# Kernel tuning notes

Hardware: AMD Instinct MI355X
Metric: run time of the kernel (lower is better)

## Reference

```python
import jax, jax.numpy as jnp
import numpy as np

EPS = 1e-6  # torch.nn.CosineSimilarity eps


def setup_inputs() -> dict:
    key = jax.random.key(0)
    k1, k2, k3, k4 = jax.random.split(key, 4)
    B, S, I, H, P = 16, 512, 512, 512, 16
    hidden = jax.random.normal(k1, (B, S, I), dtype=jnp.float32)
    # per-prototype linear weights (no bias); torch Linear stores (out, in)
    W1 = jax.random.normal(k2, (P, H, I), dtype=jnp.float32) / np.sqrt(I)
    W2 = jax.random.normal(k3, (P, H, H), dtype=jnp.float32) / np.sqrt(H)
    protos = jax.random.normal(k4, (P, H), dtype=jnp.float32)  # torch.randn(1,H) per proto
    return {"hidden": hidden, "W1": W1, "W2": W2, "protos": protos}


def reference(hidden, W1, W2, protos):
    # Batched version of the per-prototype loop:
    # layer1: ReLU(hidden @ W1[p].T) -> [B,S,P,H]
    h1 = jax.nn.relu(jnp.einsum("bsi,phi->bsph", hidden, W1))
    # layer2: ReLU(h1 @ W2[p].T) -> [B,S,P,H]
    h2 = jax.nn.relu(jnp.einsum("bsph,pgh->bspg", h1, W2))
    # cosine similarity along feature dim vs. each prototype vector
    dot = jnp.einsum("bsph,ph->bsp", h2, protos)
    xn = jnp.maximum(jnp.linalg.norm(h2, axis=-1), EPS)          # [B,S,P]
    pn = jnp.maximum(jnp.linalg.norm(protos, axis=-1), EPS)      # [P]
    cos_scores = dot / (xn * pn)                                  # [B,S,P]
    return cos_scores
```

## Files before the change

kernel.cpp:

```cpp
#include <hip/hip_runtime.h>
#include <hip/hip_bf16.h>

#define R_TOT 8192
#define DIM   512
#define NP    16
#define EPSV  1e-6f

typedef __bf16 bf16x8 __attribute__((ext_vector_type(8)));
typedef float  f32x16 __attribute__((ext_vector_type(16)));

__device__ __forceinline__ unsigned int f2bf(float f) {
  unsigned int u = __float_as_uint(f);
  return (u + 0x7FFFu + ((u >> 16) & 1u)) >> 16;
}
__device__ __forceinline__ unsigned int pack2(float a, float b) {
  return f2bf(a) | (f2bf(b) << 16);
}
__device__ __forceinline__ f32x16 zero16() {
  f32x16 z;
  #pragma unroll
  for (int i = 0; i < 16; ++i) z[i] = 0.f;
  return z;
}

__global__ void cvt_x_kernel(const float* __restrict__ X, unsigned short* __restrict__ Xb) {
  int t   = blockIdx.x * 256 + threadIdx.x;
  int row = t >> 6;
  int c   = t & 63;
  const float4* src = (const float4*)(X + (size_t)row * DIM + c * 8);
  float4 f0 = src[0], f1 = src[1];
  uint4 o;
  o.x = pack2(f0.x, f0.y);
  o.y = pack2(f0.z, f0.w);
  o.z = pack2(f1.x, f1.y);
  o.w = pack2(f1.z, f1.w);
  *(uint4*)(Xb + (size_t)row * DIM + 8 * (c ^ (row & 7))) = o;
}

__global__ void pack_w_kernel(const float* __restrict__ W, unsigned short* __restrict__ Wp) {
  int t  = blockIdx.x * 256 + threadIdx.x;
  int l  = t & 63;
  int kk = (t >> 6) & 31;
  int mt = (t >> 11) & 15;
  int p  = t >> 15;
  int row = mt * 32 + (l & 31);
  int k0  = 16 * kk + 8 * (l >> 5);
  const float4* s = (const float4*)(W + ((size_t)p * DIM + row) * DIM + k0);
  float4 f0 = s[0], f1 = s[1];
  uint4 o;
  o.x = pack2(f0.x, f0.y);
  o.y = pack2(f0.z, f0.w);
  o.z = pack2(f1.x, f1.y);
  o.w = pack2(f1.z, f1.w);
  *(uint4*)(Wp + (size_t)t * 8) = o;
}

__global__ void proto_norm_kernel(const float* __restrict__ protos, float* __restrict__ pn) {
  int p = blockIdx.x;
  int l = threadIdx.x;
  float ss = 0.f;
  #pragma unroll
  for (int k = 0; k < DIM / 64; ++k) {
    float v = protos[p * DIM + k * 64 + l];
    ss += v * v;
  }
  #pragma unroll
  for (int m = 32; m >= 1; m >>= 1) ss += __shfl_xor(ss, m, 64);
  if (l == 0) pn[p] = fmaxf(sqrtf(ss), EPSV);
}

__device__ __forceinline__ void gemm_stage32(const unsigned short* tile,
                                             const unsigned short* __restrict__ Wpk,
                                             f32x16 acc[2],
                                             int l, int l31, int h) {
  #pragma unroll
  for (int kk = 0; kk < 32; ++kk) {
    bf16x8 a = *(const bf16x8*)(Wpk + kk * 512 + l * 8);
    #pragma unroll
    for (int nt = 0; nt < 2; ++nt) {
      int token = nt * 32 + l31;
      int boff  = (32 * kk + 16 * h) ^ ((token & 7) << 4);
      bf16x8 b = *(const bf16x8*)((const char*)tile + token * 1024 + boff);
      acc[nt] = __builtin_amdgcn_mfma_f32_32x32x16_bf16(a, b, acc[nt], 0, 0, 0);
    }
  }
}

__global__ __launch_bounds__(1024) void fused_kernel(
    const unsigned short* __restrict__ Xb,
    const unsigned short* __restrict__ W1p,
    const unsigned short* __restrict__ W2p,
    const float* __restrict__ protos,
    const float* __restrict__ pn,
    float* __restrict__ out) {
  __shared__ unsigned short tile[64 * DIM];
  __shared__ float red[16][64][2];

  const int raw = blockIdx.x;
  const int bid = (raw & 7) * 256 + (raw >> 3);
  const int p   = bid >> 7;
  const int r0  = (bid & 127) << 6;
  const int tid = threadIdx.x;
  const int w   = tid >> 6;
  const int l   = tid & 63;
  const int l31 = l & 31;
  const int h   = l >> 5;

  {
    const uint4* g = (const uint4*)(Xb + (size_t)r0 * DIM);
    uint4* s = (uint4*)tile;
    #pragma unroll
    for (int it = 0; it < 4; ++it) s[tid + it * 1024] = g[tid + it * 1024];
  }
  __syncthreads();

  f32x16 acc[2];
  acc[0] = zero16();
  acc[1] = zero16();

  gemm_stage32(tile, W1p + ((size_t)p * 16 + w) * 16384, acc, l, l31, h);

  __syncthreads();

  #pragma unroll
  for (int nt = 0; nt < 2; ++nt) {
    int token = nt * 32 + l31;
    #pragma unroll
    for (int g = 0; g < 4; ++g) {
      uint2 pk;
      pk.x = pack2(fmaxf(acc[nt][4 * g + 0], 0.f), fmaxf(acc[nt][4 * g + 1], 0.f));
      pk.y = pack2(fmaxf(acc[nt][4 * g + 2], 0.f), fmaxf(acc[nt][4 * g + 3], 0.f));
      int featb = 64 * w + 16 * g + 8 * h;
      *(uint2*)((char*)tile + token * 1024 + (featb ^ ((token & 7) << 4))) = pk;
    }
  }
  __syncthreads();

  acc[0] = zero16();
  acc[1] = zero16();

  gemm_stage32(tile, W2p + ((size_t)p * 16 + w) * 16384, acc, l, l31, h);

  float4 pv[4];
  #pragma unroll
  for (int g = 0; g < 4; ++g)
    pv[g] = *(const float4*)(protos + p * DIM + 32 * w + 8 * g + 4 * h);

  #pragma unroll
  for (int nt = 0; nt < 2; ++nt) {
    float d = 0.f, ssq = 0.f;
    #pragma unroll
    for (int g = 0; g < 4; ++g)
      #pragma unroll
      for (int j = 0; j < 4; ++j) {
        float hv = fmaxf(acc[nt][4 * g + j], 0.f);
        d   += hv * ((const float*)&pv[g])[j];
        ssq += hv * hv;
      }
    d   += __shfl_xor(d, 32, 64);
    ssq += __shfl_xor(ssq, 32, 64);
    if (l < 32) {
      red[w][nt * 32 + l31][0] = d;
      red[w][nt * 32 + l31][1] = ssq;
    }
  }
  __syncthreads();

  if (tid < 64) {
    float d = 0.f, ssq = 0.f;
    #pragma unroll
    for (int ww = 0; ww < 16; ++ww) {
      d   += red[ww][tid][0];
      ssq += red[ww][tid][1];
    }
    float xn = fmaxf(sqrtf(ssq), EPSV);
    out[(size_t)(r0 + tid) * NP + p] = d / (xn * pn[p]);
  }
}

extern "C" void kernel_launch(void* const* d_in, const int* in_sizes, int n_in,
                              void* d_out, int out_size, void* d_ws, size_t ws_size,
                              hipStream_t stream) {
  const float* X      = (const float*)d_in[0];
  const float* W1     = (const float*)d_in[1];
  const float* W2     = (const float*)d_in[2];
  const float* protos = (const float*)d_in[3];
  float* out = (float*)d_out;

  unsigned short* Xb  = (unsigned short*)d_ws;
  unsigned short* W1p = Xb  + (size_t)R_TOT * DIM;
  unsigned short* W2p = W1p + (size_t)NP * DIM * DIM;
  float* pn = (float*)(W2p + (size_t)NP * DIM * DIM);

  cvt_x_kernel<<<2048, 256, 0, stream>>>(X, Xb);
  pack_w_kernel<<<2048, 256, 0, stream>>>(W1, W1p);
  pack_w_kernel<<<2048, 256, 0, stream>>>(W2, W2p);
  proto_norm_kernel<<<NP, 64, 0, stream>>>(protos, pn);
  fused_kernel<<<2048, 1024, 0, stream>>>(Xb, W1p, W2p, protos, pn, out);
}
```

Measured before the change: 177.2 us.

## Halve fused block to 512 threads with 2x2 MFMA tiles per wave

Each wave now computes two 32-row output tiles instead of one, so every B fragment read from shared memory feeds two MFMAs and LDS traffic per MFMA drops. The block shrinks from 16 to 8 waves, with launch bounds of 512 threads and a minimum of 4 blocks. The k-loop is no longer force-unrolled. Each thread now holds four accumulators, which raises register pressure and can limit occupancy. The reduction buffer shrinks to match the smaller block.

```diff
diff --git a/kernel.cpp b/kernel.cpp
--- a/kernel.cpp
+++ b/kernel.cpp
@@ -71,22 +71,28 @@
 
 __device__ __forceinline__ void gemm_stage32(const unsigned short* tile,
                                              const unsigned short* __restrict__ Wpk,
-                                             f32x16 acc[2],
+                                             f32x16 acc[2][2],
                                              int l, int l31, int h) {
-  #pragma unroll
   for (int kk = 0; kk < 32; ++kk) {
-    bf16x8 a = *(const bf16x8*)(Wpk + kk * 512 + l * 8);
+    bf16x8 a[2], b[2];
+    #pragma unroll
+    for (int mi = 0; mi < 2; ++mi)
+      a[mi] = *(const bf16x8*)(Wpk + (size_t)mi * 16384 + kk * 512 + l * 8);
     #pragma unroll
     for (int nt = 0; nt < 2; ++nt) {
       int token = nt * 32 + l31;
       int boff  = (32 * kk + 16 * h) ^ ((token & 7) << 4);
-      bf16x8 b = *(const bf16x8*)((const char*)tile + token * 1024 + boff);
-      acc[nt] = __builtin_amdgcn_mfma_f32_32x32x16_bf16(a, b, acc[nt], 0, 0, 0);
-    }
-  }
-}
-
-__global__ __launch_bounds__(1024) void fused_kernel(
+      b[nt] = *(const bf16x8*)((const char*)tile + token * 1024 + boff);
+    }
+    #pragma unroll
+    for (int mi = 0; mi < 2; ++mi)
+      #pragma unroll
+      for (int nt = 0; nt < 2; ++nt)
+        acc[mi][nt] = __builtin_amdgcn_mfma_f32_32x32x16_bf16(a[mi], b[nt], acc[mi][nt], 0, 0, 0);
+  }
+}
+
+__global__ __launch_bounds__(512, 4) void fused_kernel(
     const unsigned short* __restrict__ Xb,
     const unsigned short* __restrict__ W1p,
     const unsigned short* __restrict__ W2p,
@@ -94,7 +100,7 @@
     const float* __restrict__ pn,
     float* __restrict__ out) {
   __shared__ unsigned short tile[64 * DIM];
-  __shared__ float red[16][64][2];
+  __shared__ float red[8][64][2];
 
   const int raw = blockIdx.x;
   const int bid = (raw & 7) * 256 + (raw >> 3);
@@ -110,52 +116,57 @@
     const uint4* g = (const uint4*)(Xb + (size_t)r0 * DIM);
     uint4* s = (uint4*)tile;
     #pragma unroll
-    for (int it = 0; it < 4; ++it) s[tid + it * 1024] = g[tid + it * 1024];
-  }
-  __syncthreads();
-
-  f32x16 acc[2];
-  acc[0] = zero16();
-  acc[1] = zero16();
-
-  gemm_stage32(tile, W1p + ((size_t)p * 16 + w) * 16384, acc, l, l31, h);
-
-  __syncthreads();
-
-  #pragma unroll
-  for (int nt = 0; nt < 2; ++nt) {
-    int token = nt * 32 + l31;
-    #pragma unroll
-    for (int g = 0; g < 4; ++g) {
-      uint2 pk;
-      pk.x = pack2(fmaxf(acc[nt][4 * g + 0], 0.f), fmaxf(acc[nt][4 * g + 1], 0.f));
-      pk.y = pack2(fmaxf(acc[nt][4 * g + 2], 0.f), fmaxf(acc[nt][4 * g + 3], 0.f));
-      int featb = 64 * w + 16 * g + 8 * h;
-      *(uint2*)((char*)tile + token * 1024 + (featb ^ ((token & 7) << 4))) = pk;
-    }
-  }
-  __syncthreads();
-
-  acc[0] = zero16();
-  acc[1] = zero16();
-
-  gemm_stage32(tile, W2p + ((size_t)p * 16 + w) * 16384, acc, l, l31, h);
-
-  float4 pv[4];
-  #pragma unroll
-  for (int g = 0; g < 4; ++g)
-    pv[g] = *(const float4*)(protos + p * DIM + 32 * w + 8 * g + 4 * h);
+    for (int it = 0; it < 8; ++it) s[tid + it * 512] = g[tid + it * 512];
+  }
+  __syncthreads();
+
+  f32x16 acc[2][2];
+  #pragma unroll
+  for (int mi = 0; mi < 2; ++mi)
+    #pragma unroll
+    for (int nt = 0; nt < 2; ++nt) acc[mi][nt] = zero16();
+
+  gemm_stage32(tile, W1p + ((size_t)p * 16 + 2 * w) * 16384, acc, l, l31, h);
+
+  __syncthreads();
+
+  #pragma unroll
+  for (int mi = 0; mi < 2; ++mi)
+    #pragma unroll
+    for (int nt = 0; nt < 2; ++nt) {
+      int token = nt * 32 + l31;
+      #pragma unroll
+      for (int g = 0; g < 4; ++g) {
+        uint2 pk;
+        pk.x = pack2(fmaxf(acc[mi][nt][4 * g + 0], 0.f), fmaxf(acc[mi][nt][4 * g + 1], 0.f));
+        pk.y = pack2(fmaxf(acc[mi][nt][4 * g + 2], 0.f), fmaxf(acc[mi][nt][4 * g + 3], 0.f));
+        int featb = 128 * w + 64 * mi + 16 * g + 8 * h;
+        *(uint2*)((char*)tile + token * 1024 + (featb ^ ((token & 7) << 4))) = pk;
+      }
+    }
+  __syncthreads();
+
+  #pragma unroll
+  for (int mi = 0; mi < 2; ++mi)
+    #pragma unroll
+    for (int nt = 0; nt < 2; ++nt) acc[mi][nt] = zero16();
+
+  gemm_stage32(tile, W2p + ((size_t)p * 16 + 2 * w) * 16384, acc, l, l31, h);
 
   #pragma unroll
   for (int nt = 0; nt < 2; ++nt) {
     float d = 0.f, ssq = 0.f;
     #pragma unroll
-    for (int g = 0; g < 4; ++g)
+    for (int mi = 0; mi < 2; ++mi)
       #pragma unroll
-      for (int j = 0; j < 4; ++j) {
-        float hv = fmaxf(acc[nt][4 * g + j], 0.f);
-        d   += hv * ((const float*)&pv[g])[j];
-        ssq += hv * hv;
+      for (int g = 0; g < 4; ++g) {
+        float4 pv = *(const float4*)(protos + p * DIM + 64 * w + 32 * mi + 8 * g + 4 * h);
+        #pragma unroll
+        for (int j = 0; j < 4; ++j) {
+          float hv = fmaxf(acc[mi][nt][4 * g + j], 0.f);
+          d   += hv * ((const float*)&pv)[j];
+          ssq += hv * hv;
+        }
       }
     d   += __shfl_xor(d, 32, 64);
     ssq += __shfl_xor(ssq, 32, 64);
@@ -169,7 +180,7 @@
   if (tid < 64) {
     float d = 0.f, ssq = 0.f;
     #pragma unroll
-    for (int ww = 0; ww < 16; ++ww) {
+    for (int ww = 0; ww < 8; ++ww) {
       d   += red[ww][tid][0];
       ssq += red[ww][tid][1];
     }
@@ -196,5 +207,5 @@
   pack_w_kernel<<<2048, 256, 0, stream>>>(W1, W1p);
   pack_w_kernel<<<2048, 256, 0, stream>>>(W2, W2p);
   proto_norm_kernel<<<NP, 64, 0, stream>>>(protos, pn);
-  fused_kernel<<<2048, 1024, 0, stream>>>(Xb, W1p, W2p, protos, pn, out);
-}
+  fused_kernel<<<2048, 512, 0, stream>>>(Xb, W1p, W2p, protos, pn, out);
+}
```

Measured after the change: 165.8 us. 6.4% less time.
